# Kernel tuning notes

Measured on AMD Instinct MI355X. Metric: run time of the kernel, lower is better.

The kernel has to match this reference:

```python
import jax, jax.numpy as jnp
import numpy as np

ALIGNED_H, ALIGNED_W, ALIGNED_T = 7, 7, 4
SPATIAL_SCALE, TIME_SCALE = 1.0 / 16.0, 1.0
B, C, T, H, W = 4, 256, 16, 64, 64
N_ROIS = 1200


def setup_inputs() -> dict:
    key = jax.random.key(0)
    kf, kb, kx, ky, kw, kh, kt, kd = jax.random.split(key, 8)
    features = jax.random.normal(kf, (B, C, T, H, W), dtype=jnp.float32)
    b = jax.random.randint(kb, (N_ROIS,), 0, B).astype(jnp.float32)
    # image-space boxes (1024x1024 image, stride-16 features); temporal interval in frame units
    x1 = jax.random.uniform(kx, (N_ROIS,), minval=0.0, maxval=700.0)
    y1 = jax.random.uniform(ky, (N_ROIS,), minval=0.0, maxval=700.0)
    x2 = jnp.minimum(x1 + jax.random.uniform(kw, (N_ROIS,), minval=32.0, maxval=320.0), 1023.0)
    y2 = jnp.minimum(y1 + jax.random.uniform(kh, (N_ROIS,), minval=32.0, maxval=320.0), 1023.0)
    t1 = jax.random.uniform(kt, (N_ROIS,), minval=0.0, maxval=10.0)
    t2 = jnp.minimum(t1 + jax.random.uniform(kd, (N_ROIS,), minval=2.0, maxval=6.0), 15.0)
    rois = jnp.stack([b, x1, y1, x2, y2, t1, t2], axis=1)  # [N, 7]
    return {"features": features, "rois": rois}


def _axis_samples(start, end, size, n_out):
    # classic roi_align sampling: bin = (end - start + 1) / (n_out - 1), sample at start + i*bin
    length = jnp.maximum(end - start + 1.0, 1.0)                                  # [N]
    step = length / (n_out - 1.0)
    coord = start[:, None] + step[:, None] * jnp.arange(n_out, dtype=jnp.float32)[None, :]  # [N, n_out]
    valid = (coord >= 0.0) & (coord < size)
    lo = jnp.clip(jnp.floor(coord), 0.0, size - 1.0)
    frac = coord - lo
    lo_i = lo.astype(jnp.int32)
    hi_i = jnp.minimum(lo_i + 1, size - 1)
    return lo_i, hi_i, frac, valid.astype(jnp.float32)


def roi_align_3d(features, rois, p_t, p_h, p_w, sscale, tscale):
    Bf, Cf, Tf, Hf, Wf = features.shape
    f = jnp.transpose(features, (0, 2, 3, 4, 1))  # [B,T,H,W,C] channel-last for clean gather
    bidx = rois[:, 0].astype(jnp.int32)
    x1 = rois[:, 1] * sscale
    y1 = rois[:, 2] * sscale
    x2 = rois[:, 3] * sscale
    y2 = rois[:, 4] * sscale
    t1 = rois[:, 5] * tscale
    t2 = rois[:, 6] * tscale
    tl, th, tfr, tv = _axis_samples(t1, t2, Tf, p_t)  # [N, p_t]
    yl, yh, yfr, yv = _axis_samples(y1, y2, Hf, p_h)  # [N, p_h]
    xl, xh, xfr, xv = _axis_samples(x1, x2, Wf, p_w)  # [N, p_w]
    b4 = bidx[:, None, None, None]
    out = jnp.zeros((rois.shape[0], p_t, p_h, p_w, Cf), dtype=features.dtype)
    # trilinear interpolation: sum over 8 corners
    for ti, wt in ((tl, 1.0 - tfr), (th, tfr)):
        for yi, wy in ((yl, 1.0 - yfr), (yh, yfr)):
            for xi, wx in ((xl, 1.0 - xfr), (xh, xfr)):
                v = f[b4, ti[:, :, None, None], yi[:, None, :, None], xi[:, None, None, :]]  # [N,pt,ph,pw,C]
                w = wt[:, :, None, None] * wy[:, None, :, None] * wx[:, None, None, :]
                out = out + v * w[..., None]
    # zero out-of-bounds sample points (matches CUDA kernel behavior)
    mask = tv[:, :, None, None] * yv[:, None, :, None] * xv[:, None, None, :]
    out = out * mask[..., None]
    return jnp.transpose(out, (0, 4, 1, 2, 3))  # [N, C, p_t, p_h, p_w]


def _avg_pool3d_k2s1(x):
    s = x[..., :-1, :, :] + x[..., 1:, :, :]
    s = s[..., :, :-1, :] + s[..., :, 1:, :]
    s = s[..., :, :, :-1] + s[..., :, :, 1:]
    return s * 0.125


def reference(features, rois):
    x = roi_align_3d(features, rois, ALIGNED_T + 1, ALIGNED_H + 1, ALIGNED_W + 1,
                     SPATIAL_SCALE, TIME_SCALE)
    return _avg_pool3d_k2s1(x)  # [N, C, ALIGNED_T, ALIGNED_H, ALIGNED_W]
```

## Files before the change

### kernel.cpp

```cpp
#include <hip/hip_runtime.h>

#define C_ 256
#define T_ 16
#define H_ 64
#define W_ 64
#define PT 5
#define PH 8
#define PW 8
#define OT 4
#define OH 7
#define OW 7
#define SSCALE (1.0f/16.0f)
#define TSCALE 1.0f
#define NP (PT * PH * PW)
#define CG 32
#define PSTR 321

typedef float f4v __attribute__((ext_vector_type(4)));

__global__ __launch_bounds__(256) void transpose_kernel(const float* __restrict__ f,
                                                        float* __restrict__ ft) {
    __shared__ float tile[64][65];
    const int THW = T_ * H_ * W_;
    int thw0 = blockIdx.x * 64;
    int c0 = blockIdx.y * 64;
    int b = blockIdx.z;
    int l4 = threadIdx.x & 15;
    int row = threadIdx.x >> 4;
#pragma unroll
    for (int k = 0; k < 4; ++k) {
        int c = row + k * 16;
        const f4v* src = reinterpret_cast<const f4v*>(
            &f[((size_t)b * C_ + c0 + c) * THW + thw0 + l4 * 4]);
        f4v v = __builtin_nontemporal_load(src);
        tile[c][l4 * 4 + 0] = v[0];
        tile[c][l4 * 4 + 1] = v[1];
        tile[c][l4 * 4 + 2] = v[2];
        tile[c][l4 * 4 + 3] = v[3];
    }
    __syncthreads();
#pragma unroll
    for (int k = 0; k < 4; ++k) {
        int t = row + k * 16;
        f4v v;
        v[0] = tile[l4 * 4 + 0][t];
        v[1] = tile[l4 * 4 + 1][t];
        v[2] = tile[l4 * 4 + 2][t];
        v[3] = tile[l4 * 4 + 3][t];
        *reinterpret_cast<f4v*>(&ft[((size_t)b * THW + thw0 + t) * C_ + c0 + l4 * 4]) = v;
    }
}

__global__ __launch_bounds__(256) void roi_kernel(const float* __restrict__ ft,
                                                  const float* __restrict__ rois,
                                                  float* __restrict__ out) {
    __shared__ float smp[CG][PSTR];
    __shared__ float sroi[7];
    __shared__ int s_lo[21], s_hi[21];
    __shared__ float s_fr[21], s_vd[21];

    int r = blockIdx.y;
    int c0 = blockIdx.x * CG;

    if (threadIdx.x < 7) sroi[threadIdx.x] = rois[r * 7 + threadIdx.x];
    __syncthreads();

    if (threadIdx.x < 21) {
        int i = threadIdx.x;
        float start, end, size;
        int j, n;
        if (i < 5) {
            j = i; n = PT;
            start = sroi[5] * TSCALE; end = sroi[6] * TSCALE; size = (float)T_;
        } else if (i < 13) {
            j = i - 5; n = PH;
            start = sroi[2] * SSCALE; end = sroi[4] * SSCALE; size = (float)H_;
        } else {
            j = i - 13; n = PW;
            start = sroi[1] * SSCALE; end = sroi[3] * SSCALE; size = (float)W_;
        }
        float length = fmaxf(end - start + 1.0f, 1.0f);
        float step = length / (float)(n - 1);
        float coord = start + step * (float)j;
        float valid = (coord >= 0.0f && coord < size) ? 1.0f : 0.0f;
        float lo = fminf(fmaxf(floorf(coord), 0.0f), size - 1.0f);
        s_lo[i] = (int)lo;
        s_hi[i] = min((int)lo + 1, (int)size - 1);
        s_fr[i] = coord - lo;
        s_vd[i] = valid;
    }
    __syncthreads();

    int b = (int)sroi[0];
    int c4 = threadIdx.x & 7;
    int psub = threadIdx.x >> 3;
    const int CQ = C_ / 4;
    const f4v* fb = reinterpret_cast<const f4v*>(ft)
                  + (size_t)b * (T_ * H_ * W_) * CQ + (c0 >> 2) + c4;

#pragma unroll 2
    for (int it = 0; it < NP / 32; ++it) {
        int p = it * 32 + psub;
        int ti = p >> 6;
        int yi = (p >> 3) & 7;
        int xi = p & 7;
        int tl = s_lo[ti], th = s_hi[ti];
        float tf = s_fr[ti];
        int yl = s_lo[5 + yi], yh = s_hi[5 + yi];
        float fy = s_fr[5 + yi];
        int xl = s_lo[13 + xi], xh = s_hi[13 + xi];
        float fx = s_fr[13 + xi];
        float mask = s_vd[ti] * s_vd[5 + yi] * s_vd[13 + xi];

        int r_tl_yl = (tl * H_ + yl) * W_;
        int r_tl_yh = (tl * H_ + yh) * W_;
        int r_th_yl = (th * H_ + yl) * W_;
        int r_th_yh = (th * H_ + yh) * W_;

        f4v v000 = fb[(r_tl_yl + xl) * CQ];
        f4v v001 = fb[(r_tl_yl + xh) * CQ];
        f4v v010 = fb[(r_tl_yh + xl) * CQ];
        f4v v011 = fb[(r_tl_yh + xh) * CQ];
        f4v v100 = fb[(r_th_yl + xl) * CQ];
        f4v v101 = fb[(r_th_yl + xh) * CQ];
        f4v v110 = fb[(r_th_yh + xl) * CQ];
        f4v v111 = fb[(r_th_yh + xh) * CQ];

        f4v vx00 = v000 + fx * (v001 - v000);
        f4v vx01 = v010 + fx * (v011 - v010);
        f4v vx10 = v100 + fx * (v101 - v100);
        f4v vx11 = v110 + fx * (v111 - v110);
        f4v vy0 = vx00 + fy * (vx01 - vx00);
        f4v vy1 = vx10 + fy * (vx11 - vx10);
        f4v v = vy0 + tf * (vy1 - vy0);
        v *= mask;

        int cb = c4 * 4;
        smp[cb + 0][p] = v[0];
        smp[cb + 1][p] = v[1];
        smp[cb + 2][p] = v[2];
        smp[cb + 3][p] = v[3];
    }
    __syncthreads();

    const int NOUT = CG * OT * OH * OW;
    float* outc = out + ((size_t)r * C_ + c0) * (OT * OH * OW);
    for (int ov = 0; ov < (NOUT + 255) / 256; ++ov) {
        int o = ov * 256 + threadIdx.x;
        if (o < NOUT) {
            int cc = o / 196;
            int pos = o - cc * 196;
            int t = pos / 49;
            int rem = pos - t * 49;
            int h = rem / 7;
            int w = rem - h * 7;
            const float* s0 = &smp[cc][t * 64 + h * 8 + w];
            float s = s0[0] + s0[1] + s0[8] + s0[9] + s0[64] + s0[65] + s0[72] + s0[73];
            __builtin_nontemporal_store(s * 0.125f, &outc[o]);
        }
    }
}

__device__ __forceinline__ void axis_sample(float start, float end, float size, int n,
                                            int j, int& lo_i, int& hi_i, float& frac,
                                            float& valid) {
    float length = fmaxf(end - start + 1.0f, 1.0f);
    float step = length / (float)(n - 1);
    float coord = start + step * (float)j;
    valid = (coord >= 0.0f && coord < size) ? 1.0f : 0.0f;
    float lo = fminf(fmaxf(floorf(coord), 0.0f), size - 1.0f);
    frac = coord - lo;
    lo_i = (int)lo;
    hi_i = min(lo_i + 1, (int)size - 1);
}

__global__ void roi_direct(const float* __restrict__ f, const float* __restrict__ rois,
                           float* __restrict__ out, long long total) {
    long long idx = (long long)blockIdx.x * 256 + threadIdx.x;
    if (idx >= total) return;
    int w = (int)(idx % OW);
    long long q = idx / OW;
    int h = (int)(q % OH);
    q /= OH;
    int t = (int)(q % OT);
    q /= OT;
    int c = (int)(q % C_);
    int r = (int)(q / C_);

    float rb = rois[r * 7 + 0];
    float x1 = rois[r * 7 + 1] * SSCALE;
    float y1 = rois[r * 7 + 2] * SSCALE;
    float x2 = rois[r * 7 + 3] * SSCALE;
    float y2 = rois[r * 7 + 4] * SSCALE;
    float t1 = rois[r * 7 + 5] * TSCALE;
    float t2 = rois[r * 7 + 6] * TSCALE;
    int b = (int)rb;
    const float* fc = f + ((size_t)b * C_ + c) * (T_ * H_ * W_);

    float acc = 0.0f;
    for (int dt = 0; dt < 2; ++dt) {
        int tlo, thi; float tf, tv;
        axis_sample(t1, t2, (float)T_, PT, t + dt, tlo, thi, tf, tv);
        for (int dh = 0; dh < 2; ++dh) {
            int ylo, yhi; float yf, yv;
            axis_sample(y1, y2, (float)H_, PH, h + dh, ylo, yhi, yf, yv);
            for (int dw = 0; dw < 2; ++dw) {
                int xlo, xhi; float xf, xv;
                axis_sample(x1, x2, (float)W_, PW, w + dw, xlo, xhi, xf, xv);
                float v000 = fc[(tlo * H_ + ylo) * W_ + xlo];
                float v001 = fc[(tlo * H_ + ylo) * W_ + xhi];
                float v010 = fc[(tlo * H_ + yhi) * W_ + xlo];
                float v011 = fc[(tlo * H_ + yhi) * W_ + xhi];
                float v100 = fc[(thi * H_ + ylo) * W_ + xlo];
                float v101 = fc[(thi * H_ + ylo) * W_ + xhi];
                float v110 = fc[(thi * H_ + yhi) * W_ + xlo];
                float v111 = fc[(thi * H_ + yhi) * W_ + xhi];
                float vx00 = v000 + xf * (v001 - v000);
                float vx01 = v010 + xf * (v011 - v010);
                float vx10 = v100 + xf * (v101 - v100);
                float vx11 = v110 + xf * (v111 - v110);
                float vy0 = vx00 + yf * (vx01 - vx00);
                float vy1 = vx10 + yf * (vx11 - vx10);
                float v = vy0 + tf * (vy1 - vy0);
                acc += v * (tv * yv * xv);
            }
        }
    }
    out[idx] = acc * 0.125f;
}

extern "C" void kernel_launch(void* const* d_in, const int* in_sizes, int n_in,
                              void* d_out, int out_size, void* d_ws, size_t ws_size,
                              hipStream_t stream) {
    const float* feat = (const float*)d_in[0];
    const float* rois = (const float*)d_in[1];
    float* out = (float*)d_out;
    int nroi = in_sizes[1] / 7;
    int B = in_sizes[0] / (C_ * T_ * H_ * W_);
    size_t need = (size_t)B * T_ * H_ * W_ * C_ * sizeof(float);

    if (ws_size >= need) {
        dim3 g1(T_ * H_ * W_ / 64, C_ / 64, B);
        transpose_kernel<<<g1, 256, 0, stream>>>(feat, (float*)d_ws);
        dim3 g2(C_ / CG, nroi);
        roi_kernel<<<g2, 256, 0, stream>>>((const float*)d_ws, rois, out);
    } else {
        long long total = (long long)nroi * C_ * OT * OH * OW;
        roi_direct<<<(int)((total + 255) / 256), 256, 0, stream>>>(feat, rois, out, total);
    }
}
```

Baseline: 615.4 us.

## Stream time slices through double-buffered LDS and fold weights into precomputed offsets

```diff
diff --git a/kernel.cpp b/kernel.cpp
--- a/kernel.cpp
+++ b/kernel.cpp
@@ -12,11 +12,11 @@
 #define OW 7
 #define SSCALE (1.0f/16.0f)
 #define TSCALE 1.0f
-#define NP (PT * PH * PW)
 #define CG 32
-#define PSTR 321
+#define LROW 66
 
 typedef float f4v __attribute__((ext_vector_type(4)));
+typedef float f2v __attribute__((ext_vector_type(2)));
 
 __global__ __launch_bounds__(256) void transpose_kernel(const float* __restrict__ f,
                                                         float* __restrict__ ft) {
@@ -51,13 +51,14 @@
     }
 }
 
-__global__ __launch_bounds__(256) void roi_kernel(const float* __restrict__ ft,
-                                                  const float* __restrict__ rois,
-                                                  float* __restrict__ out) {
-    __shared__ float smp[CG][PSTR];
+__global__ __launch_bounds__(256, 6) void roi_kernel(const float* __restrict__ ft,
+                                                     const float* __restrict__ rois,
+                                                     float* __restrict__ out) {
+    __shared__ float smp[2][CG][LROW];
     __shared__ float sroi[7];
-    __shared__ int s_lo[21], s_hi[21];
-    __shared__ float s_fr[21], s_vd[21];
+    __shared__ int2 s_trow[PT]; __shared__ float2 s_twt[PT];
+    __shared__ int2 s_yrow[PH]; __shared__ float2 s_ywt[PH];
+    __shared__ int2 s_xoff[PW]; __shared__ float2 s_xwt[PW];
 
     int r = blockIdx.y;
     int c0 = blockIdx.x * CG;
@@ -68,96 +69,102 @@
     if (threadIdx.x < 21) {
         int i = threadIdx.x;
         float start, end, size;
-        int j, n;
+        int j, n, scale;
         if (i < 5) {
             j = i; n = PT;
-            start = sroi[5] * TSCALE; end = sroi[6] * TSCALE; size = (float)T_;
+            start = sroi[5] * TSCALE; end = sroi[6] * TSCALE;
+            size = (float)T_; scale = H_ * W_ * C_ * 4;
         } else if (i < 13) {
             j = i - 5; n = PH;
-            start = sroi[2] * SSCALE; end = sroi[4] * SSCALE; size = (float)H_;
+            start = sroi[2] * SSCALE; end = sroi[4] * SSCALE;
+            size = (float)H_; scale = W_ * C_ * 4;
         } else {
             j = i - 13; n = PW;
-            start = sroi[1] * SSCALE; end = sroi[3] * SSCALE; size = (float)W_;
+            start = sroi[1] * SSCALE; end = sroi[3] * SSCALE;
+            size = (float)W_; scale = C_ * 4;
         }
         float length = fmaxf(end - start + 1.0f, 1.0f);
         float step = length / (float)(n - 1);
         float coord = start + step * (float)j;
         float valid = (coord >= 0.0f && coord < size) ? 1.0f : 0.0f;
         float lo = fminf(fmaxf(floorf(coord), 0.0f), size - 1.0f);
-        s_lo[i] = (int)lo;
-        s_hi[i] = min((int)lo + 1, (int)size - 1);
-        s_fr[i] = coord - lo;
-        s_vd[i] = valid;
+        int lo_i = (int)lo;
+        int hi_i = min(lo_i + 1, (int)size - 1);
+        float fr = coord - lo;
+        int2 offs; offs.x = lo_i * scale; offs.y = hi_i * scale;
+        float2 wts; wts.x = (1.0f - fr) * valid; wts.y = fr * valid;
+        if (i < 5)       { s_trow[j] = offs; s_twt[j] = wts; }
+        else if (i < 13) { s_yrow[j] = offs; s_ywt[j] = wts; }
+        else             { s_xoff[j] = offs; s_xwt[j] = wts; }
     }
     __syncthreads();
 
     int b = (int)sroi[0];
     int c4 = threadIdx.x & 7;
-    int psub = threadIdx.x >> 3;
-    const int CQ = C_ / 4;
-    const f4v* fb = reinterpret_cast<const f4v*>(ft)
-                  + (size_t)b * (T_ * H_ * W_) * CQ + (c0 >> 2) + c4;
-
-#pragma unroll 2
-    for (int it = 0; it < NP / 32; ++it) {
-        int p = it * 32 + psub;
-        int ti = p >> 6;
-        int yi = (p >> 3) & 7;
-        int xi = p & 7;
-        int tl = s_lo[ti], th = s_hi[ti];
-        float tf = s_fr[ti];
-        int yl = s_lo[5 + yi], yh = s_hi[5 + yi];
-        float fy = s_fr[5 + yi];
-        int xl = s_lo[13 + xi], xh = s_hi[13 + xi];
-        float fx = s_fr[13 + xi];
-        float mask = s_vd[ti] * s_vd[5 + yi] * s_vd[13 + xi];
-
-        int r_tl_yl = (tl * H_ + yl) * W_;
-        int r_tl_yh = (tl * H_ + yh) * W_;
-        int r_th_yl = (th * H_ + yl) * W_;
-        int r_th_yh = (th * H_ + yh) * W_;
-
-        f4v v000 = fb[(r_tl_yl + xl) * CQ];
-        f4v v001 = fb[(r_tl_yl + xh) * CQ];
-        f4v v010 = fb[(r_tl_yh + xl) * CQ];
-        f4v v011 = fb[(r_tl_yh + xh) * CQ];
-        f4v v100 = fb[(r_th_yl + xl) * CQ];
-        f4v v101 = fb[(r_th_yl + xh) * CQ];
-        f4v v110 = fb[(r_th_yh + xl) * CQ];
-        f4v v111 = fb[(r_th_yh + xh) * CQ];
-
-        f4v vx00 = v000 + fx * (v001 - v000);
-        f4v vx01 = v010 + fx * (v011 - v010);
-        f4v vx10 = v100 + fx * (v101 - v100);
-        f4v vx11 = v110 + fx * (v111 - v110);
-        f4v vy0 = vx00 + fy * (vx01 - vx00);
-        f4v vy1 = vx10 + fy * (vx11 - vx10);
-        f4v v = vy0 + tf * (vy1 - vy0);
-        v *= mask;
-
-        int cb = c4 * 4;
-        smp[cb + 0][p] = v[0];
-        smp[cb + 1][p] = v[1];
-        smp[cb + 2][p] = v[2];
-        smp[cb + 3][p] = v[3];
-    }
-    __syncthreads();
-
-    const int NOUT = CG * OT * OH * OW;
-    float* outc = out + ((size_t)r * C_ + c0) * (OT * OH * OW);
-    for (int ov = 0; ov < (NOUT + 255) / 256; ++ov) {
-        int o = ov * 256 + threadIdx.x;
-        if (o < NOUT) {
-            int cc = o / 196;
-            int pos = o - cc * 196;
-            int t = pos / 49;
-            int rem = pos - t * 49;
-            int h = rem / 7;
-            int w = rem - h * 7;
-            const float* s0 = &smp[cc][t * 64 + h * 8 + w];
-            float s = s0[0] + s0[1] + s0[8] + s0[9] + s0[64] + s0[65] + s0[72] + s0[73];
-            __builtin_nontemporal_store(s * 0.125f, &outc[o]);
-        }
+    int slot = threadIdx.x >> 3;
+    const char* fb = (const char*)ft
+        + ((size_t)b * (T_ * H_ * W_ * C_) + (size_t)(c0 + c4 * 4)) * 4;
+
+    for (int t = 0; t < PT; ++t) {
+        int2 tr = s_trow[t];
+        float2 tw = s_twt[t];
+        float (*buf)[LROW] = smp[t & 1];
+#pragma unroll
+        for (int k = 0; k < 2; ++k) {
+            int yx = slot + k * 32;
+            int y = yx >> 3, x = yx & 7;
+            int2 yr = s_yrow[y]; float2 yw = s_ywt[y];
+            int2 xo = s_xoff[x]; float2 xw = s_xwt[x];
+            int rA = tr.x + yr.x;
+            int rB = tr.x + yr.y;
+            int rC = tr.y + yr.x;
+            int rD = tr.y + yr.y;
+            float wA = tw.x * yw.x, wB = tw.x * yw.y;
+            float wC = tw.y * yw.x, wD = tw.y * yw.y;
+            f4v a0 = *(const f4v*)(fb + rA + xo.x);
+            f4v a1 = *(const f4v*)(fb + rA + xo.y);
+            f4v b0 = *(const f4v*)(fb + rB + xo.x);
+            f4v b1 = *(const f4v*)(fb + rB + xo.y);
+            f4v e0 = *(const f4v*)(fb + rC + xo.x);
+            f4v e1 = *(const f4v*)(fb + rC + xo.y);
+            f4v d0 = *(const f4v*)(fb + rD + xo.x);
+            f4v d1 = *(const f4v*)(fb + rD + xo.y);
+            f4v vl = wA * a0 + wB * b0 + wC * e0 + wD * d0;
+            f4v vh = wA * a1 + wB * b1 + wC * e1 + wD * d1;
+            f4v v = xw.x * vl + xw.y * vh;
+            float* col = &buf[c4 * 4][yx];
+            col[0 * LROW] = v[0];
+            col[1 * LROW] = v[1];
+            col[2 * LROW] = v[2];
+            col[3 * LROW] = v[3];
+        }
+        __syncthreads();
+
+        if (t > 0) {
+            int cc = threadIdx.x & 31;
+            int hh = threadIdx.x >> 5;
+            if (hh < 7) {
+                const float* pa = &smp[(t - 1) & 1][cc][hh * 8];
+                const float* pb = &smp[t & 1][cc][hh * 8];
+                float s8[8];
+#pragma unroll
+                for (int x2 = 0; x2 < 4; ++x2) {
+                    f2v alo = *(const f2v*)(pa + 2 * x2);
+                    f2v ahi = *(const f2v*)(pa + 8 + 2 * x2);
+                    f2v blo = *(const f2v*)(pb + 2 * x2);
+                    f2v bhi = *(const f2v*)(pb + 8 + 2 * x2);
+                    f2v s = (alo + ahi) + (blo + bhi);
+                    s8[2 * x2] = s[0];
+                    s8[2 * x2 + 1] = s[1];
+                }
+                float* op = out + ((size_t)r * C_ + c0 + cc) * (OT * OH * OW)
+                          + (t - 1) * (OH * OW) + hh * OW;
+#pragma unroll
+                for (int w = 0; w < 7; ++w)
+                    __builtin_nontemporal_store((s8[w] + s8[w + 1]) * 0.125f, op + w);
+            }
+        }
+        __syncthreads();
     }
 }
 
```

Measured after the change: 946.4 us. 1.54x slower.
